# Optimization experiments

Hardware: AMD Instinct MI355X
Metric: run time of the kernel (lower is better)

Reference implementation:

```python
import jax, jax.numpy as jnp
import numpy as np

N, L, D, H, DFF = 16, 192, 512, 8, 2048
HD = D // H


def _mha(q, k, v, wq, bq, wk, bk, wv, bv, wo, bo, mask=None):
    # q: [B, Lq, D], k/v: [B, Lk, D]
    B, Lq, _ = q.shape
    def proj(x, W, b):
        y = x @ W + b
        return y.reshape(B, -1, H, HD).transpose(0, 2, 1, 3)  # [B, H, L, HD]
    Q, K, V = proj(q, wq, bq), proj(k, wk, bk), proj(v, wv, bv)
    QK = jnp.einsum('bhqd,bhkd->bhqk', Q, K) / jnp.sqrt(jnp.asarray(HD, Q.dtype))
    if mask is not None:
        QK = QK + (1.0 - mask) * (-1e9)
    A = jax.nn.softmax(QK, axis=-1)
    out = jnp.einsum('bhqk,bhkd->bhqd', A, V).transpose(0, 2, 1, 3).reshape(B, Lq, D)
    return out @ wo + bo


def _ln(x, g, b, eps=1e-6):
    mu = x.mean(-1, keepdims=True)
    var = ((x - mu) ** 2).mean(-1, keepdims=True)
    return (x - mu) / jnp.sqrt(var + eps) * g + b


def setup_inputs() -> dict:
    key = jax.random.key(0)
    ks = jax.random.split(key, 16)
    w = lambda k, sh: jax.random.normal(k, sh, jnp.float32) * 0.02
    inp = {
        'S': jax.random.normal(ks[0], (N, L, D), jnp.float32),
        'padding_mask': jax.random.randint(ks[1], (N * N, 1, 1, L), 0, 2, dtype=jnp.int32),
        'training': 0,
    }
    for i, nm in enumerate(['ca_wq', 'ca_wk', 'ca_wv', 'ca_wo', 'ia_wq', 'ia_wk', 'ia_wv', 'ia_wo']):
        inp[nm] = w(ks[2 + i], (D, D))
        inp[nm.replace('w', 'b')] = jnp.zeros((D,), jnp.float32)
    inp['ffn_w1'] = w(ks[10], (D, DFF)); inp['ffn_b1'] = jnp.zeros((DFF,), jnp.float32)
    inp['ffn_w2'] = w(ks[11], (DFF, D)); inp['ffn_b2'] = jnp.zeros((D,), jnp.float32)
    inp['ln1_g'] = jnp.ones((D,), jnp.float32); inp['ln1_b'] = jnp.zeros((D,), jnp.float32)
    inp['ln2_g'] = jnp.ones((D,), jnp.float32); inp['ln2_b'] = jnp.zeros((D,), jnp.float32)
    return inp


def reference(S, ca_wq, ca_bq, ca_wk, ca_bk, ca_wv, ca_bv, ca_wo, ca_bo,
              ia_wq, ia_bq, ia_wk, ia_bk, ia_wv, ia_bv, ia_wo, ia_bo,
              ffn_w1, ffn_b1, ffn_w2, ffn_b2, ln1_g, ln1_b, ln2_g, ln2_b,
              padding_mask, training):
    # training == 0 -> dropout layers are identity (inference mode)
    mask = padding_mask.astype(S.dtype)
    n, l, d = S.shape
    # all-pairs cross attention: query seq i attends to key/value seq j
    queries = jnp.repeat(S, n, axis=0)   # [n*n, l, d]
    keyvalue = jnp.tile(S, (n, 1, 1))    # [n*n, l, d]
    S_attn = _mha(queries, keyvalue, keyvalue,
                  ca_wq, ca_bq, ca_wk, ca_bk, ca_wv, ca_bv, ca_wo, ca_bo, mask=mask)
    S_attn = S_attn.reshape(n, n, l, d).transpose(1, 2, 0, 3).reshape(n * l, n, d)
    S_flip = S.reshape(n * l, 1, d)
    S_attn = _mha(S_flip, S_attn, S_attn,
                  ia_wq, ia_bq, ia_wk, ia_bk, ia_wv, ia_bv, ia_wo, ia_bo)
    S_attn = S_attn.reshape(n, l, d)
    S_norm = _ln(S + S_attn, ln1_g, ln1_b)
    S_ffn = jax.nn.relu(S_norm @ ffn_w1 + ffn_b1) @ ffn_w2 + ffn_b2
    return _ln(S_norm + S_ffn, ln2_g, ln2_b)
```

## Files before the change

### kernel.cpp

```cpp
#include <hip/hip_runtime.h>


using u16 = unsigned short;
using u32 = unsigned int;
typedef __attribute__((ext_vector_type(8))) short short8;
typedef __attribute__((ext_vector_type(4))) float f32x4;

__device__ __forceinline__ u32 cvtpk(float lo, float hi) {
  u32 r;
  asm("v_cvt_pk_bf16_f32 %0, %1, %2" : "=v"(r) : "v"(lo), "v"(hi));
  return r;
}
__device__ __forceinline__ u16 f2bf(float f) { return (u16)cvtpk(f, f); }
__device__ __forceinline__ float bf2f(u16 h) {
  return __uint_as_float(((u32)h) << 16);
}
__device__ __forceinline__ f32x4 mfma16(short8 a, short8 b, f32x4 c) {
  return __builtin_amdgcn_mfma_f32_16x16x32_bf16(a, b, c, 0, 0, 0);
}
__device__ __forceinline__ void gload16(const void* g, u16* l) {
  __builtin_amdgcn_global_load_lds(
      (const __attribute__((address_space(1))) void*)g,
      (__attribute__((address_space(3))) void*)l, 16, 0, 0);
}

template<int ROWS, int NT>
__device__ __forceinline__ void stage_g16(u16* lds, const u16* __restrict__ src,
                                          int ld, int tid) {
  constexpr int UNITS = ROWS * 8;
  constexpr int WV = NT / 64;
  int lane = tid & 63, w = tid >> 6;
  #pragma unroll
  for (int u = 0; u < UNITS / NT; ++u) {
    int base = (u * WV + w) * 64;
    int unit = base + lane;
    int row = unit >> 3, co = unit & 7;
    gload16(src + (long)row * ld + ((co ^ (row & 7)) << 3), lds + base * 8);
  }
}
template<int ROWS, int NT>
__device__ __forceinline__ void stage_f32(u16* lds, const float* __restrict__ src,
                                          int ld, int tid) {
  constexpr int UNITS = ROWS * 8;
  #pragma unroll
  for (int u = 0; u < UNITS / NT; ++u) {
    int unit = tid + u * NT;
    int row = unit >> 3, co = unit & 7;
    const float* g = src + (long)row * ld + (co << 3);
    float4 a = *(const float4*)g;
    float4 b = *(const float4*)(g + 4);
    u32 p[4] = {cvtpk(a.x, a.y), cvtpk(a.z, a.w),
                cvtpk(b.x, b.y), cvtpk(b.z, b.w)};
    *(uint4*)&lds[(row << 6) + ((co ^ (row & 7)) << 3)] = *(const uint4*)p;
  }
}

template<typename AT, typename BT, int BM, int BN, int WM, int WN>
__device__ __forceinline__ void gemm_core(const AT* __restrict__ A, int lda,
                                          const BT* __restrict__ Bt, int ldb, int K,
                                          u16* As, u16* Bs,
                                          f32x4 (&acc)[BM / (WM * 16)][BN / (WN * 16)]) {
  constexpr int NT = WM * WN * 64;
  constexpr int MI = BM / (WM * 16), NJ = BN / (WN * 16);
  int tid = threadIdx.x, lane = tid & 63, wid = tid >> 6;
  int wr = wid % WM, wc = wid / WM;
  int g = lane >> 4, c = lane & 15;
  #pragma unroll
  for (int mi = 0; mi < MI; ++mi)
    #pragma unroll
    for (int nj = 0; nj < NJ; ++nj)
      acc[mi][nj] = f32x4{0.f, 0.f, 0.f, 0.f};
  for (int kb = 0; kb < K; kb += 64) {
    __syncthreads();
    if constexpr (sizeof(AT) == 4) stage_f32<BM, NT>(As, A + kb, lda, tid);
    else                           stage_g16<BM, NT>(As, A + kb, lda, tid);
    if constexpr (sizeof(BT) == 4) stage_f32<BN, NT>(Bs, Bt + kb, ldb, tid);
    else                           stage_g16<BN, NT>(Bs, Bt + kb, ldb, tid);
    __syncthreads();
    #pragma unroll
    for (int kk = 0; kk < 2; ++kk) {
      int sl = ((kk * 4 + g) ^ (c & 7)) << 3;
      short8 af[MI], bfr[NJ];
      #pragma unroll
      for (int mi = 0; mi < MI; ++mi)
        af[mi] = *(const short8*)&As[((wr * (BM / WM) + mi * 16 + c) << 6) + sl];
      #pragma unroll
      for (int nj = 0; nj < NJ; ++nj)
        bfr[nj] = *(const short8*)&Bs[((wc * (BN / WN) + nj * 16 + c) << 6) + sl];
      #pragma unroll
      for (int mi = 0; mi < MI; ++mi)
        #pragma unroll
        for (int nj = 0; nj < NJ; ++nj)
          acc[mi][nj] = mfma16(af[mi], bfr[nj], acc[mi][nj]);
    }
  }
}

struct TJob { const float* src; u16* dst; int R, C, tile0; };
struct TJobs { TJob j[9]; };

__global__ __launch_bounds__(256) void k_transpose(TJobs jobs) {
  __shared__ float tile[32][33];
  int t = blockIdx.x;
  int ji = 0;
  #pragma unroll
  for (int k = 1; k < 9; ++k)
    if (t >= jobs.j[k].tile0) ji = k;
  TJob jb = jobs.j[ji];
  int lt = t - jb.tile0;
  int tpr = jb.C >> 5;
  int tr = lt / tpr, tc = lt % tpr;
  int tid = threadIdx.x;
  #pragma unroll
  for (int u = 0; u < 4; ++u) {
    int e = tid + u * 256;
    int r = e >> 5, cc = e & 31;
    tile[r][cc] = jb.src[(long)(tr * 32 + r) * jb.C + tc * 32 + cc];
  }
  __syncthreads();
  #pragma unroll
  for (int u = 0; u < 4; ++u) {
    int e = tid + u * 256;
    int r = e >> 5, cc = e & 31;
    jb.dst[(long)(tc * 32 + r) * jb.R + tr * 32 + cc] = f2bf(tile[cc][r]);
  }
}

__global__ __launch_bounds__(256) void k_qkv(const float* __restrict__ S,
    const u16* __restrict__ bt0, const u16* __restrict__ bt1,
    const u16* __restrict__ bt2, const u16* __restrict__ bt3,
    const float* __restrict__ b0, const float* __restrict__ b1,
    const float* __restrict__ b2, const float* __restrict__ b3,
    u16* __restrict__ Qc, u16* __restrict__ Kc, u16* __restrict__ Vt,
    u16* __restrict__ Qi) {
  __shared__ u16 As[128 * 64];
  __shared__ u16 Bs[128 * 64];
  int f = blockIdx.x;
  int swz = (f & 7) * 12 + (f >> 3);
  int mb = swz >> 2, nb = swz & 3, z = blockIdx.y;
  const u16* bt = z == 0 ? bt0 : z == 1 ? bt1 : z == 2 ? bt2 : bt3;
  const float* bias = z == 0 ? b0 : z == 1 ? b1 : z == 2 ? b2 : b3;
  f32x4 acc[4][4];
  gemm_core<float, u16, 128, 128, 2, 2>(S + (long)mb * 128 * 512, 512,
                                        bt + (long)nb * 128 * 512, 512, 512,
                                        As, Bs, acc);
  int lane = threadIdx.x & 63, wid = threadIdx.x >> 6;
  int wr = wid & 1, wc = wid >> 1, g = lane >> 4, cl = lane & 15;
  #pragma unroll
  for (int mi = 0; mi < 4; ++mi)
    #pragma unroll
    for (int nj = 0; nj < 4; ++nj)
      #pragma unroll
      for (int r = 0; r < 4; ++r) {
        int row = mb * 128 + wr * 64 + mi * 16 + g * 4 + r;
        int col = nb * 128 + wc * 64 + nj * 16 + cl;
        float v = acc[mi][nj][r] + bias[col];
        int seq = row / 192, t = row % 192, h = col >> 6, hd = col & 63;
        if (z == 0)      Qc[((long)(seq * 8 + h) * 192 + t) * 64 + hd] = f2bf(v * 0.125f);
        else if (z == 1) Kc[((long)(seq * 8 + h) * 192 + t) * 64 + hd] = f2bf(v);
        else if (z == 2) Vt[((long)(seq * 8 + h) * 64 + hd) * 192 + t] = f2bf(v);
        else             Qi[(long)row * 512 + col] = f2bf(v * 0.125f);
      }
}

__global__ __launch_bounds__(256) void k_attn_ca(const u16* __restrict__ Qc,
    const u16* __restrict__ Kc, const u16* __restrict__ VtG,
    const int* __restrict__ mask, u16* __restrict__ AC) {
  __shared__ u16 Ks[192 * 64];
  __shared__ u16 Vs[64 * 192];
  __shared__ __align__(16) float mbf[192];
  int bh = blockIdx.x;
  int b = bh >> 3, h = bh & 7;
  int i = b >> 4, j = b & 15;
  int tid = threadIdx.x, lane = tid & 63, w = tid >> 6;
  int g = lane >> 4, c = lane & 15;
  int qb = w * 48;

  const u16* Kbase = Kc + (long)(j * 8 + h) * 192 * 64;
  #pragma unroll
  for (int u = 0; u < 6; ++u) {
    int base = (u * 4 + w) * 64;
    int unit = base + lane;
    int row = unit >> 3, co = unit & 7;
    gload16(Kbase + (long)row * 64 + ((co ^ (row & 7)) << 3), Ks + base * 8);
  }
  const u16* Vbase = VtG + (long)(j * 8 + h) * 64 * 192;
  #pragma unroll
  for (int u = 0; u < 6; ++u) {
    int base = (u * 4 + w) * 64;
    int unit = base + lane;
    int row = unit / 24, co = unit - row * 24;
    gload16(Vbase + (long)row * 192 + ((co ^ (row & 7)) << 3), Vs + base * 8);
  }
  short8 bq[3][2];
  const u16* Qbase = Qc + (long)(i * 8 + h) * 192 * 64;
  #pragma unroll
  for (int nj = 0; nj < 3; ++nj)
    #pragma unroll
    for (int ks = 0; ks < 2; ++ks)
      bq[nj][ks] = *(const short8*)(Qbase + (long)(qb + nj * 16 + c) * 64 + ks * 32 + g * 8);
  if (tid < 192) mbf[tid] = mask[(long)b * 192 + tid] ? 0.f : -1e9f;
  __syncthreads();

  f32x4 oa[4][3];
  #pragma unroll
  for (int mi = 0; mi < 4; ++mi)
    #pragma unroll
    for (int nj = 0; nj < 3; ++nj)
      oa[mi][nj] = f32x4{0.f, 0.f, 0.f, 0.f};
  float sm[3] = {0.f, 0.f, 0.f};
  int srcLo = c | ((g & 1) << 5);
  int srcHi = srcLo + 16;
  int hi = g & 2;

  for (int s = 0; s < 6; ++s) {
    short8 ak[2][2];
    #pragma unroll
    for (int kh = 0; kh < 2; ++kh) {
      int row = (2 * s + kh) * 16 + c;
      #pragma unroll
      for (int ks = 0; ks < 2; ++ks)
        ak[kh][ks] = *(const short8*)&Ks[(row << 6) + (((ks * 4 + g) ^ (c & 7)) << 3)];
    }
    f32x4 sa[2][3];
    __builtin_amdgcn_s_setprio(1);
    #pragma unroll
    for (int kh = 0; kh < 2; ++kh)
      #pragma unroll
      for (int nj = 0; nj < 3; ++nj) {
        sa[kh][nj] = mfma16(ak[kh][0], bq[nj][0], f32x4{0.f, 0.f, 0.f, 0.f});
        sa[kh][nj] = mfma16(ak[kh][1], bq[nj][1], sa[kh][nj]);
      }
    __builtin_amdgcn_s_setprio(0);
    u32 pk[2][3][2];
    #pragma unroll
    for (int kh = 0; kh < 2; ++kh) {
      f32x4 m4 = *(const f32x4*)&mbf[(2 * s + kh) * 16 + g * 4];
      #pragma unroll
      for (int nj = 0; nj < 3; ++nj) {
        float p0 = __expf(sa[kh][nj][0] + m4[0]);
        float p1 = __expf(sa[kh][nj][1] + m4[1]);
        float p2 = __expf(sa[kh][nj][2] + m4[2]);
        float p3 = __expf(sa[kh][nj][3] + m4[3]);
        sm[nj] += (p0 + p1) + (p2 + p3);
        pk[kh][nj][0] = cvtpk(p0, p1);
        pk[kh][nj][1] = cvtpk(p2, p3);
      }
    }
    short8 bfg[3];
    #pragma unroll
    for (int nj = 0; nj < 3; ++nj) {
      u32 w0a = (u32)__shfl((int)pk[0][nj][0], srcLo);
      u32 w0b = (u32)__shfl((int)pk[1][nj][0], srcLo);
      u32 w1a = (u32)__shfl((int)pk[0][nj][1], srcLo);
      u32 w1b = (u32)__shfl((int)pk[1][nj][1], srcLo);
      u32 w2a = (u32)__shfl((int)pk[0][nj][0], srcHi);
      u32 w2b = (u32)__shfl((int)pk[1][nj][0], srcHi);
      u32 w3a = (u32)__shfl((int)pk[0][nj][1], srcHi);
      u32 w3b = (u32)__shfl((int)pk[1][nj][1], srcHi);
      union { u32 u[4]; short8 s8; } bf;
      bf.u[0] = hi ? w0b : w0a;
      bf.u[1] = hi ? w1b : w1a;
      bf.u[2] = hi ? w2b : w2a;
      bf.u[3] = hi ? w3b : w3a;
      bfg[nj] = bf.s8;
    }
    int sl = ((s * 4 + g) ^ (c & 7)) << 3;
    __builtin_amdgcn_s_setprio(1);
    #pragma unroll
    for (int mi = 0; mi < 4; ++mi) {
      short8 av = *(const short8*)&Vs[(mi * 16 + c) * 192 + sl];
      #pragma unroll
      for (int nj = 0; nj < 3; ++nj)
        oa[mi][nj] = mfma16(av, bfg[nj], oa[mi][nj]);
    }
    __builtin_amdgcn_s_setprio(0);
  }
  #pragma unroll
  for (int nj = 0; nj < 3; ++nj) {
    sm[nj] += __shfl_xor(sm[nj], 16);
    sm[nj] += __shfl_xor(sm[nj], 32);
  }
  #pragma unroll
  for (int nj = 0; nj < 3; ++nj) {
    float rs = 1.0f / sm[nj];
    int q = qb + nj * 16 + c;
    u16* dst = AC + ((long)(b * 192 + q)) * 512 + h * 64 + g * 4;
    #pragma unroll
    for (int mi = 0; mi < 4; ++mi) {
      u32 p2[2] = {cvtpk(oa[mi][nj][0] * rs, oa[mi][nj][1] * rs),
                   cvtpk(oa[mi][nj][2] * rs, oa[mi][nj][3] * rs)};
      *(uint2*)(dst + mi * 16) = *(const uint2*)p2;
    }
  }
}

__global__ __launch_bounds__(256) void k_oproj_ca(const u16* __restrict__ AC,
    const u16* __restrict__ woT, const float* __restrict__ bo,
    u16* __restrict__ S2) {
  __shared__ u16 As[128 * 64];
  __shared__ u16 Bs[128 * 64];
  int f = blockIdx.x;
  int swz = (f & 7) * 192 + (f >> 3);
  int mb = swz >> 2, nb = swz & 3;
  f32x4 acc[4][4];
  gemm_core<u16, u16, 128, 128, 2, 2>(AC + (long)mb * 128 * 512, 512,
                                      woT + (long)nb * 128 * 512, 512, 512,
                                      As, Bs, acc);
  int lane = threadIdx.x & 63, wid = threadIdx.x >> 6;
  int wr = wid & 1, wc = wid >> 1, g = lane >> 4, cl = lane & 15;
  #pragma unroll
  for (int mi = 0; mi < 4; ++mi)
    #pragma unroll
    for (int nj = 0; nj < 4; ++nj)
      #pragma unroll
      for (int r = 0; r < 4; ++r) {
        int row = mb * 128 + wr * 64 + mi * 16 + g * 4 + r;
        int col = nb * 128 + wc * 64 + nj * 16 + cl;
        S2[(long)row * 512 + col] = f2bf(acc[mi][nj][r] + bo[col]);
      }
}

__global__ __launch_bounds__(256) void k_uproj(const u16* __restrict__ Qi,
    const float* __restrict__ wk, u16* __restrict__ U) {
  __shared__ u16 As[128 * 64];
  __shared__ u16 Bs[128 * 64];
  int mb = blockIdx.x, nb = blockIdx.y, h = blockIdx.z;
  f32x4 acc[4][4];
  gemm_core<u16, float, 128, 128, 2, 2>(Qi + (long)mb * 128 * 512 + h * 64, 512,
                                        wk + (long)nb * 128 * 512 + h * 64, 512, 64,
                                        As, Bs, acc);
  int lane = threadIdx.x & 63, wid = threadIdx.x >> 6;
  int wr = wid & 1, wc = wid >> 1, g = lane >> 4, cl = lane & 15;
  #pragma unroll
  for (int mi = 0; mi < 4; ++mi)
    #pragma unroll
    for (int nj = 0; nj < 4; ++nj)
      #pragma unroll
      for (int r = 0; r < 4; ++r) {
        int row = mb * 128 + wr * 64 + mi * 16 + g * 4 + r;
        int col = nb * 128 + wc * 64 + nj * 16 + cl;
        U[((long)row * 8 + h) * 512 + col] = f2bf(acc[mi][nj][r]);
      }
}

__global__ __launch_bounds__(256) void k_ia_attn(const u16* __restrict__ S2,
    const u16* __restrict__ U, const u16* __restrict__ Qi,
    const float* __restrict__ bk, u16* __restrict__ Y) {
  __shared__ u16 s2[16 * 520];
  __shared__ float Lp[4][16][17];
  __shared__ float aL[8][16];
  __shared__ float cL[8];
  int tok = blockIdx.x;
  int tid = threadIdx.x, lane = tid & 63, w = tid >> 6;
  {
    const u16* src = S2 + (long)tok * 512;
    #pragma unroll
    for (int u = 0; u < 4; ++u) {
      int e = tid + u * 256;
      int r = e >> 6, cc = (e & 63) << 3;
      *(uint4*)&s2[r * 520 + cc] = *(const uint4*)(src + (long)r * 3072 * 512 + cc);
    }
  }
  if (w == 0) {
    int h = lane >> 3, p = lane & 7;
    short8 qv = *(const short8*)(Qi + (long)tok * 512 + h * 64 + p * 8);
    const float* bkp = bk + h * 64 + p * 8;
    float s = 0.f;
    #pragma unroll
    for (int v = 0; v < 8; ++v) s += bf2f((u16)qv[v]) * bkp[v];
    s += __shfl_xor(s, 1); s += __shfl_xor(s, 2); s += __shfl_xor(s, 4);
    if (p == 0) cL[h] = s;
  }
  __syncthreads();
  {
    int g = lane >> 4, c = lane & 15;
    const u16* Ub = U + (long)tok * 4096 + (long)(c & 7) * 512;
    f32x4 accL = {0.f, 0.f, 0.f, 0.f};
    #pragma unroll
    for (int kk = 0; kk < 4; ++kk) {
      int d = w * 128 + kk * 32 + g * 8;
      short8 aS = *(const short8*)&s2[c * 520 + d];
      short8 bU = *(const short8*)(Ub + d);
      accL = mfma16(aS, bU, accL);
    }
    #pragma unroll
    for (int r = 0; r < 4; ++r) Lp[w][g * 4 + r][c] = accL[r];
  }
  __syncthreads();
  if (w == 0) {
    int h = lane & 7, i0 = lane >> 3;
    float L0 = Lp[0][i0][h] + Lp[1][i0][h] + Lp[2][i0][h] + Lp[3][i0][h] + cL[h];
    float L1 = Lp[0][i0 + 8][h] + Lp[1][i0 + 8][h] + Lp[2][i0 + 8][h] +
               Lp[3][i0 + 8][h] + cL[h];
    float e0 = __expf(L0), e1 = __expf(L1);
    float s = e0 + e1;
    s += __shfl_xor(s, 8); s += __shfl_xor(s, 16); s += __shfl_xor(s, 32);
    float rs = 1.0f / s;
    aL[h][i0] = e0 * rs;
    aL[h][i0 + 8] = e1 * rs;
  }
  __syncthreads();
  {
    int h = tid & 7, d0 = (tid >> 3) << 4;
    float y[16];
    #pragma unroll
    for (int v = 0; v < 16; ++v) y[v] = 0.f;
    #pragma unroll
    for (int i = 0; i < 16; ++i) {
      float a = aL[h][i];
      short8 v0 = *(const short8*)&s2[i * 520 + d0];
      short8 v1 = *(const short8*)&s2[i * 520 + d0 + 8];
      #pragma unroll
      for (int v = 0; v < 8; ++v) {
        y[v]     += a * bf2f((u16)v0[v]);
        y[8 + v] += a * bf2f((u16)v1[v]);
      }
    }
    u32 o[8];
    #pragma unroll
    for (int v = 0; v < 8; ++v) o[v] = cvtpk(y[2 * v], y[2 * v + 1]);
    u16* dst = Y + ((long)tok * 8 + h) * 512 + d0;
    *(uint4*)dst = *(const uint4*)&o[0];
    *(uint4*)(dst + 8) = *(const uint4*)&o[4];
  }
}

__global__ __launch_bounds__(256) void k_vapply(const u16* __restrict__ Y,
    const u16* __restrict__ wvT, const float* __restrict__ bv,
    u16* __restrict__ AO) {
  __shared__ u16 As[128 * 64];
  __shared__ u16 Bs[64 * 64];
  int mb = blockIdx.x, h = blockIdx.z;
  f32x4 acc[2][4];
  gemm_core<u16, u16, 128, 64, 4, 1>(Y + (long)mb * 128 * 4096 + h * 512, 4096,
                                     wvT + (long)h * 64 * 512, 512, 512,
                                     As, Bs, acc);
  int lane = threadIdx.x & 63, wid = threadIdx.x >> 6;
  int g = lane >> 4, cl = lane & 15;
  #pragma unroll
  for (int mi = 0; mi < 2; ++mi)
    #pragma unroll
    for (int nj = 0; nj < 4; ++nj)
      #pragma unroll
      for (int r = 0; r < 4; ++r) {
        int row = mb * 128 + wid * 32 + mi * 16 + g * 4 + r;
        int col = h * 64 + nj * 16 + cl;
        AO[(long)row * 512 + col] = f2bf(acc[mi][nj][r] + bv[col]);
      }
}

__global__ __launch_bounds__(256) void k_gemm_f32out(const u16* __restrict__ A, int K,
    const u16* __restrict__ BT, const float* __restrict__ bias,
    float* __restrict__ out) {
  __shared__ u16 As[128 * 64];
  __shared__ u16 Bs[64 * 64];
  int f = blockIdx.x;
  int swz = (f & 7) * 24 + (f >> 3);
  int mb = swz >> 3, nb = swz & 7;
  f32x4 acc[4][2];
  gemm_core<u16, u16, 128, 64, 2, 2>(A + (long)mb * 128 * K, K,
                                     BT + (long)nb * 64 * K, K, K, As, Bs, acc);
  int lane = threadIdx.x & 63, wid = threadIdx.x >> 6;
  int wr = wid & 1, wc = wid >> 1, g = lane >> 4, cl = lane & 15;
  #pragma unroll
  for (int mi = 0; mi < 4; ++mi)
    #pragma unroll
    for (int nj = 0; nj < 2; ++nj)
      #pragma unroll
      for (int r = 0; r < 4; ++r) {
        int row = mb * 128 + wr * 64 + mi * 16 + g * 4 + r;
        int col = nb * 64 + wc * 32 + nj * 16 + cl;
        out[(long)row * 512 + col] = acc[mi][nj][r] + bias[col];
      }
}

__global__ __launch_bounds__(256) void k_ffn1(const u16* __restrict__ A,
    const u16* __restrict__ BT, const float* __restrict__ bias,
    u16* __restrict__ out) {
  __shared__ u16 As[128 * 64];
  __shared__ u16 Bs[128 * 64];
  int f = blockIdx.x;
  int swz = (f & 7) * 48 + (f >> 3);
  int mb = swz >> 4, nb = swz & 15;
  f32x4 acc[4][4];
  gemm_core<u16, u16, 128, 128, 2, 2>(A + (long)mb * 128 * 512, 512,
                                      BT + (long)nb * 128 * 512, 512, 512,
                                      As, Bs, acc);
  int lane = threadIdx.x & 63, wid = threadIdx.x >> 6;
  int wr = wid & 1, wc = wid >> 1, g = lane >> 4, cl = lane & 15;
  #pragma unroll
  for (int mi = 0; mi < 4; ++mi)
    #pragma unroll
    for (int nj = 0; nj < 4; ++nj)
      #pragma unroll
      for (int r = 0; r < 4; ++r) {
        int row = mb * 128 + wr * 64 + mi * 16 + g * 4 + r;
        int col = nb * 128 + wc * 64 + nj * 16 + cl;
        out[(long)row * 2048 + col] = f2bf(fmaxf(acc[mi][nj][r] + bias[col], 0.f));
      }
}

__global__ __launch_bounds__(256) void k_ln(const float* __restrict__ X1,
    const float* __restrict__ X2, const float* __restrict__ gg,
    const float* __restrict__ bb, float* __restrict__ outF,
    u16* __restrict__ outB) {
  __shared__ float red[8];
  int row = blockIdx.x, tid = threadIdx.x;
  long base = (long)row * 512;
  float x0 = X1[base + tid] + X2[base + tid];
  float x1 = X1[base + tid + 256] + X2[base + tid + 256];
  float s = x0 + x1, ss = x0 * x0 + x1 * x1;
  #pragma unroll
  for (int m = 1; m <= 32; m <<= 1) {
    s += __shfl_xor(s, m);
    ss += __shfl_xor(ss, m);
  }
  int w = tid >> 6;
  if ((tid & 63) == 0) { red[w] = s; red[4 + w] = ss; }
  __syncthreads();
  s = red[0] + red[1] + red[2] + red[3];
  ss = red[4] + red[5] + red[6] + red[7];
  float mu = s * (1.0f / 512.0f);
  float var = ss * (1.0f / 512.0f) - mu * mu;
  float rstd = 1.0f / sqrtf(var + 1e-6f);
  float y0 = (x0 - mu) * rstd * gg[tid] + bb[tid];
  float y1 = (x1 - mu) * rstd * gg[tid + 256] + bb[tid + 256];
  if (outF) { outF[base + tid] = y0; outF[base + tid + 256] = y1; }
  if (outB) { outB[base + tid] = f2bf(y0); outB[base + tid + 256] = f2bf(y1); }
}

extern "C" void kernel_launch(void* const* d_in, const int* in_sizes, int n_in,
                              void* d_out, int out_size, void* d_ws, size_t ws_size,
                              hipStream_t stream) {
  const float* S      = (const float*)d_in[0];
  const int*   maskp  = (const int*)d_in[1];
  const float* ca_wq  = (const float*)d_in[3];
  const float* ca_bq  = (const float*)d_in[4];
  const float* ca_wk  = (const float*)d_in[5];
  const float* ca_bk  = (const float*)d_in[6];
  const float* ca_wv  = (const float*)d_in[7];
  const float* ca_bv  = (const float*)d_in[8];
  const float* ca_wo  = (const float*)d_in[9];
  const float* ca_bo  = (const float*)d_in[10];
  const float* ia_wq  = (const float*)d_in[11];
  const float* ia_bq  = (const float*)d_in[12];
  const float* ia_wk  = (const float*)d_in[13];
  const float* ia_bk  = (const float*)d_in[14];
  const float* ia_wv  = (const float*)d_in[15];
  const float* ia_bv  = (const float*)d_in[16];
  const float* ia_wo  = (const float*)d_in[17];
  const float* ia_bo  = (const float*)d_in[18];
  const float* ffn_w1 = (const float*)d_in[19];
  const float* ffn_b1 = (const float*)d_in[20];
  const float* ffn_w2 = (const float*)d_in[21];
  const float* ffn_b2 = (const float*)d_in[22];
  const float* ln1_g  = (const float*)d_in[23];
  const float* ln1_b  = (const float*)d_in[24];
  const float* ln2_g  = (const float*)d_in[25];
  const float* ln2_b  = (const float*)d_in[26];

  char* ws = (char*)d_ws;
  constexpr size_t OFF_WQT  = 0;
  constexpr size_t OFF_WKT  = 524288;
  constexpr size_t OFF_WVT  = 1048576;
  constexpr size_t OFF_IQT  = 1572864;
  constexpr size_t OFF_WOTC = 2097152;
  constexpr size_t OFF_WVTI = 2621440;
  constexpr size_t OFF_WOTI = 3145728;
  constexpr size_t OFF_W1T  = 3670016;
  constexpr size_t OFF_W2T  = 5767168;
  constexpr size_t OFF_QC   = 7864320;
  constexpr size_t OFF_KC   = 11010048;
  constexpr size_t OFF_VT   = 14155776;
  constexpr size_t OFF_QI   = 17301504;
  constexpr size_t OFF_AC   = 20447232;
  constexpr size_t OFF_S2   = 70778880;
  constexpr size_t OFF_U    = OFF_AC;
  constexpr size_t OFF_Y    = OFF_AC + 25165824;
  constexpr size_t OFF_AO   = OFF_QI;
  constexpr size_t OFF_IAO  = OFF_QC;
  constexpr size_t OFF_SNB  = OFF_VT;
  constexpr size_t OFF_SNF  = OFF_S2;
  constexpr size_t OFF_HFF  = OFF_S2 + 6291456;
  constexpr size_t OFF_FFO  = OFF_HFF + 12582912;

  u16* wqT  = (u16*)(ws + OFF_WQT);
  u16* wkT  = (u16*)(ws + OFF_WKT);
  u16* wvT  = (u16*)(ws + OFF_WVT);
  u16* iqT  = (u16*)(ws + OFF_IQT);
  u16* woTc = (u16*)(ws + OFF_WOTC);
  u16* wvTi = (u16*)(ws + OFF_WVTI);
  u16* woTi = (u16*)(ws + OFF_WOTI);
  u16* w1T  = (u16*)(ws + OFF_W1T);
  u16* w2T  = (u16*)(ws + OFF_W2T);
  u16* Qc   = (u16*)(ws + OFF_QC);
  u16* Kc   = (u16*)(ws + OFF_KC);
  u16* Vt   = (u16*)(ws + OFF_VT);
  u16* Qi   = (u16*)(ws + OFF_QI);
  u16* AC   = (u16*)(ws + OFF_AC);
  u16* S2   = (u16*)(ws + OFF_S2);
  u16* U    = (u16*)(ws + OFF_U);
  u16* Y    = (u16*)(ws + OFF_Y);
  u16* AO   = (u16*)(ws + OFF_AO);
  float* IAO = (float*)(ws + OFF_IAO);
  u16* SNB  = (u16*)(ws + OFF_SNB);
  float* SNF = (float*)(ws + OFF_SNF);
  u16* HFF  = (u16*)(ws + OFF_HFF);
  float* FFO = (float*)(ws + OFF_FFO);

  TJobs tj;
  int t0 = 0;
  auto SET = [&](int k, const float* s, u16* d, int R, int C) {
    tj.j[k].src = s; tj.j[k].dst = d; tj.j[k].R = R; tj.j[k].C = C; tj.j[k].tile0 = t0;
    t0 += (R / 32) * (C / 32);
  };
  SET(0, ca_wq, wqT, 512, 512);
  SET(1, ca_wk, wkT, 512, 512);
  SET(2, ca_wv, wvT, 512, 512);
  SET(3, ia_wq, iqT, 512, 512);
  SET(4, ca_wo, woTc, 512, 512);
  SET(5, ia_wv, wvTi, 512, 512);
  SET(6, ia_wo, woTi, 512, 512);
  SET(7, ffn_w1, w1T, 512, 2048);
  SET(8, ffn_w2, w2T, 2048, 512);

  k_transpose<<<dim3(t0), 256, 0, stream>>>(tj);
  k_qkv<<<dim3(96, 4), 256, 0, stream>>>(S, wqT, wkT, wvT, iqT,
                                         ca_bq, ca_bk, ca_bv, ia_bq,
                                         Qc, Kc, Vt, Qi);
  k_attn_ca<<<dim3(2048), 256, 0, stream>>>(Qc, Kc, Vt, maskp, AC);
  k_oproj_ca<<<dim3(1536), 256, 0, stream>>>(AC, woTc, ca_bo, S2);
  k_uproj<<<dim3(24, 4, 8), 256, 0, stream>>>(Qi, ia_wk, U);
  k_ia_attn<<<dim3(3072), 256, 0, stream>>>(S2, U, Qi, ia_bk, Y);
  k_vapply<<<dim3(24, 1, 8), 256, 0, stream>>>(Y, wvTi, ia_bv, AO);
  k_gemm_f32out<<<dim3(192), 256, 0, stream>>>(AO, 512, woTi, ia_bo, IAO);
  k_ln<<<dim3(3072), 256, 0, stream>>>(S, IAO, ln1_g, ln1_b, SNF, SNB);
  k_ffn1<<<dim3(384), 256, 0, stream>>>(SNB, w1T, ffn_b1, HFF);
  k_gemm_f32out<<<dim3(192), 256, 0, stream>>>(HFF, 2048, w2T, ffn_b2, FFO);
  k_ln<<<dim3(3072), 256, 0, stream>>>(SNF, FFO, ln2_g, ln2_b, (float*)d_out, nullptr);
}
```

Baseline: 210.8 us.

## Pre-cast S to bf16, merge QKV launches, co-schedule attention with U projection

Adds a kernel that casts S to bf16 once, so the QKV GEMM reads bf16 instead of converting fp32 in each of its four z-slices. The four projection weights are stored contiguously and k_qkv runs as one 1D grid over all 16 column blocks. When the workspace is large enough, the cross-attention blocks and the U-projection GEMM blocks share one launch, removing a kernel boundary and filling idle CUs. The cost is an extra cast kernel, a larger workspace footprint, and a merged kernel that needs the larger shared-memory allocation for both paths.

```diff
diff --git a/kernel.cpp b/kernel.cpp
--- a/kernel.cpp
+++ b/kernel.cpp
@@ -96,6 +96,16 @@
   }
 }
 
+__global__ __launch_bounds__(256) void k_cast(const float* __restrict__ S,
+                                              u16* __restrict__ Sb) {
+  int idx = (blockIdx.x * 256 + threadIdx.x) * 8;
+  float4 a = *(const float4*)(S + idx);
+  float4 b = *(const float4*)(S + idx + 4);
+  u32 p[4] = {cvtpk(a.x, a.y), cvtpk(a.z, a.w),
+              cvtpk(b.x, b.y), cvtpk(b.z, b.w)};
+  *(uint4*)(Sb + idx) = *(const uint4*)p;
+}
+
 struct TJob { const float* src; u16* dst; int R, C, tile0; };
 struct TJobs { TJob j[9]; };
 
@@ -126,24 +136,23 @@
   }
 }
 
-__global__ __launch_bounds__(256) void k_qkv(const float* __restrict__ S,
-    const u16* __restrict__ bt0, const u16* __restrict__ bt1,
-    const u16* __restrict__ bt2, const u16* __restrict__ bt3,
+__global__ __launch_bounds__(256) void k_qkv(const u16* __restrict__ Sb,
+    const u16* __restrict__ btAll,
     const float* __restrict__ b0, const float* __restrict__ b1,
     const float* __restrict__ b2, const float* __restrict__ b3,
     u16* __restrict__ Qc, u16* __restrict__ Kc, u16* __restrict__ Vt,
     u16* __restrict__ Qi) {
-  __shared__ u16 As[128 * 64];
-  __shared__ u16 Bs[128 * 64];
+  __shared__ u16 SH[16384];
   int f = blockIdx.x;
-  int swz = (f & 7) * 12 + (f >> 3);
-  int mb = swz >> 2, nb = swz & 3, z = blockIdx.y;
-  const u16* bt = z == 0 ? bt0 : z == 1 ? bt1 : z == 2 ? bt2 : bt3;
+  int swz = (f & 7) * 48 + (f >> 3);
+  int mb = swz >> 4, nb = swz & 15;
+  f32x4 acc[4][4];
+  gemm_core<u16, u16, 128, 128, 2, 2>(Sb + (long)mb * 128 * 512, 512,
+                                      btAll + (long)nb * 128 * 512, 512, 512,
+                                      SH, SH + 8192, acc);
+  int z = nb >> 2;
   const float* bias = z == 0 ? b0 : z == 1 ? b1 : z == 2 ? b2 : b3;
-  f32x4 acc[4][4];
-  gemm_core<float, u16, 128, 128, 2, 2>(S + (long)mb * 128 * 512, 512,
-                                        bt + (long)nb * 128 * 512, 512, 512,
-                                        As, Bs, acc);
+  float scale = (z == 0 || z == 3) ? 0.125f : 1.0f;
   int lane = threadIdx.x & 63, wid = threadIdx.x >> 6;
   int wr = wid & 1, wc = wid >> 1, g = lane >> 4, cl = lane & 15;
   #pragma unroll
@@ -153,145 +162,171 @@
       #pragma unroll
       for (int r = 0; r < 4; ++r) {
         int row = mb * 128 + wr * 64 + mi * 16 + g * 4 + r;
-        int col = nb * 128 + wc * 64 + nj * 16 + cl;
-        float v = acc[mi][nj][r] + bias[col];
-        int seq = row / 192, t = row % 192, h = col >> 6, hd = col & 63;
-        if (z == 0)      Qc[((long)(seq * 8 + h) * 192 + t) * 64 + hd] = f2bf(v * 0.125f);
+        int cz = (nb & 3) * 128 + wc * 64 + nj * 16 + cl;
+        float v = (acc[mi][nj][r] + bias[cz]) * scale;
+        int seq = row / 192, t = row % 192, h = cz >> 6, hd = cz & 63;
+        if (z == 0)      Qc[((long)(seq * 8 + h) * 192 + t) * 64 + hd] = f2bf(v);
         else if (z == 1) Kc[((long)(seq * 8 + h) * 192 + t) * 64 + hd] = f2bf(v);
         else if (z == 2) Vt[((long)(seq * 8 + h) * 64 + hd) * 192 + t] = f2bf(v);
-        else             Qi[(long)row * 512 + col] = f2bf(v * 0.125f);
-      }
-}
-
-__global__ __launch_bounds__(256) void k_attn_ca(const u16* __restrict__ Qc,
+        else             Qi[(long)row * 512 + cz] = f2bf(v);
+      }
+}
+
+__global__ __launch_bounds__(256) void k_attn_up(const u16* __restrict__ Qc,
     const u16* __restrict__ Kc, const u16* __restrict__ VtG,
-    const int* __restrict__ mask, u16* __restrict__ AC) {
-  __shared__ u16 Ks[192 * 64];
-  __shared__ u16 Vs[64 * 192];
-  __shared__ __align__(16) float mbf[192];
-  int bh = blockIdx.x;
-  int b = bh >> 3, h = bh & 7;
-  int i = b >> 4, j = b & 15;
+    const int* __restrict__ mask, u16* __restrict__ AC,
+    const u16* __restrict__ Qi, const float* __restrict__ wk,
+    u16* __restrict__ U, int attnBlocks) {
+  __shared__ __align__(16) u16 SH[24960];
+  int bid = blockIdx.x;
   int tid = threadIdx.x, lane = tid & 63, w = tid >> 6;
   int g = lane >> 4, c = lane & 15;
-  int qb = w * 48;
-
-  const u16* Kbase = Kc + (long)(j * 8 + h) * 192 * 64;
-  #pragma unroll
-  for (int u = 0; u < 6; ++u) {
-    int base = (u * 4 + w) * 64;
-    int unit = base + lane;
-    int row = unit >> 3, co = unit & 7;
-    gload16(Kbase + (long)row * 64 + ((co ^ (row & 7)) << 3), Ks + base * 8);
-  }
-  const u16* Vbase = VtG + (long)(j * 8 + h) * 64 * 192;
-  #pragma unroll
-  for (int u = 0; u < 6; ++u) {
-    int base = (u * 4 + w) * 64;
-    int unit = base + lane;
-    int row = unit / 24, co = unit - row * 24;
-    gload16(Vbase + (long)row * 192 + ((co ^ (row & 7)) << 3), Vs + base * 8);
-  }
-  short8 bq[3][2];
-  const u16* Qbase = Qc + (long)(i * 8 + h) * 192 * 64;
-  #pragma unroll
-  for (int nj = 0; nj < 3; ++nj)
-    #pragma unroll
-    for (int ks = 0; ks < 2; ++ks)
-      bq[nj][ks] = *(const short8*)(Qbase + (long)(qb + nj * 16 + c) * 64 + ks * 32 + g * 8);
-  if (tid < 192) mbf[tid] = mask[(long)b * 192 + tid] ? 0.f : -1e9f;
-  __syncthreads();
-
-  f32x4 oa[4][3];
-  #pragma unroll
-  for (int mi = 0; mi < 4; ++mi)
+  if (bid < attnBlocks) {
+    u16* Ks = SH;
+    u16* Vs = SH + 12288;
+    float* mbf = (float*)(SH + 24576);
+    int b = bid >> 3, h = bid & 7;
+    int i = b >> 4, j = b & 15;
+    int qb = w * 48;
+
+    const u16* Kbase = Kc + (long)(j * 8 + h) * 192 * 64;
+    #pragma unroll
+    for (int u = 0; u < 6; ++u) {
+      int base = (u * 4 + w) * 64;
+      int unit = base + lane;
+      int row = unit >> 3, co = unit & 7;
+      gload16(Kbase + (long)row * 64 + ((co ^ (row & 7)) << 3), Ks + base * 8);
+    }
+    const u16* Vbase = VtG + (long)(j * 8 + h) * 64 * 192;
+    #pragma unroll
+    for (int u = 0; u < 6; ++u) {
+      int base = (u * 4 + w) * 64;
+      int unit = base + lane;
+      int row = unit / 24, co = unit - row * 24;
+      gload16(Vbase + (long)row * 192 + ((co ^ (row & 7)) << 3), Vs + base * 8);
+    }
+    short8 bq[3][2];
+    const u16* Qbase = Qc + (long)(i * 8 + h) * 192 * 64;
     #pragma unroll
     for (int nj = 0; nj < 3; ++nj)
-      oa[mi][nj] = f32x4{0.f, 0.f, 0.f, 0.f};
-  float sm[3] = {0.f, 0.f, 0.f};
-  int srcLo = c | ((g & 1) << 5);
-  int srcHi = srcLo + 16;
-  int hi = g & 2;
-
-  for (int s = 0; s < 6; ++s) {
-    short8 ak[2][2];
-    #pragma unroll
-    for (int kh = 0; kh < 2; ++kh) {
-      int row = (2 * s + kh) * 16 + c;
       #pragma unroll
       for (int ks = 0; ks < 2; ++ks)
-        ak[kh][ks] = *(const short8*)&Ks[(row << 6) + (((ks * 4 + g) ^ (c & 7)) << 3)];
-    }
-    f32x4 sa[2][3];
-    __builtin_amdgcn_s_setprio(1);
-    #pragma unroll
-    for (int kh = 0; kh < 2; ++kh)
+        bq[nj][ks] = *(const short8*)(Qbase + (long)(qb + nj * 16 + c) * 64 + ks * 32 + g * 8);
+    if (tid < 192) mbf[tid] = mask[(long)b * 192 + tid] ? 0.f : -1e9f;
+    __syncthreads();
+
+    f32x4 oa[4][3];
+    #pragma unroll
+    for (int mi = 0; mi < 4; ++mi)
+      #pragma unroll
+      for (int nj = 0; nj < 3; ++nj)
+        oa[mi][nj] = f32x4{0.f, 0.f, 0.f, 0.f};
+    float sm[3] = {0.f, 0.f, 0.f};
+    int srcLo = c | ((g & 1) << 5);
+    int srcHi = srcLo + 16;
+    int hi = g & 2;
+
+    for (int s = 0; s < 6; ++s) {
+      short8 ak[2][2];
+      #pragma unroll
+      for (int kh = 0; kh < 2; ++kh) {
+        int row = (2 * s + kh) * 16 + c;
+        #pragma unroll
+        for (int ks = 0; ks < 2; ++ks)
+          ak[kh][ks] = *(const short8*)&Ks[(row << 6) + (((ks * 4 + g) ^ (c & 7)) << 3)];
+      }
+      f32x4 sa[2][3];
+      __builtin_amdgcn_s_setprio(1);
+      #pragma unroll
+      for (int kh = 0; kh < 2; ++kh)
+        #pragma unroll
+        for (int nj = 0; nj < 3; ++nj) {
+          sa[kh][nj] = mfma16(ak[kh][0], bq[nj][0], f32x4{0.f, 0.f, 0.f, 0.f});
+          sa[kh][nj] = mfma16(ak[kh][1], bq[nj][1], sa[kh][nj]);
+        }
+      __builtin_amdgcn_s_setprio(0);
+      u32 pk[2][3][2];
+      #pragma unroll
+      for (int kh = 0; kh < 2; ++kh) {
+        f32x4 m4 = *(const f32x4*)&mbf[(2 * s + kh) * 16 + g * 4];
+        #pragma unroll
+        for (int nj = 0; nj < 3; ++nj) {
+          float p0 = __expf(sa[kh][nj][0] + m4[0]);
+          float p1 = __expf(sa[kh][nj][1] + m4[1]);
+          float p2 = __expf(sa[kh][nj][2] + m4[2]);
+          float p3 = __expf(sa[kh][nj][3] + m4[3]);
+          sm[nj] += (p0 + p1) + (p2 + p3);
+          pk[kh][nj][0] = cvtpk(p0, p1);
+          pk[kh][nj][1] = cvtpk(p2, p3);
+        }
+      }
+      short8 bfg[3];
       #pragma unroll
       for (int nj = 0; nj < 3; ++nj) {
-        sa[kh][nj] = mfma16(ak[kh][0], bq[nj][0], f32x4{0.f, 0.f, 0.f, 0.f});
-        sa[kh][nj] = mfma16(ak[kh][1], bq[nj][1], sa[kh][nj]);
-      }
-    __builtin_amdgcn_s_setprio(0);
-    u32 pk[2][3][2];
-    #pragma unroll
-    for (int kh = 0; kh < 2; ++kh) {
-      f32x4 m4 = *(const f32x4*)&mbf[(2 * s + kh) * 16 + g * 4];
-      #pragma unroll
-      for (int nj = 0; nj < 3; ++nj) {
-        float p0 = __expf(sa[kh][nj][0] + m4[0]);
-        float p1 = __expf(sa[kh][nj][1] + m4[1]);
-        float p2 = __expf(sa[kh][nj][2] + m4[2]);
-        float p3 = __expf(sa[kh][nj][3] + m4[3]);
-        sm[nj] += (p0 + p1) + (p2 + p3);
-        pk[kh][nj][0] = cvtpk(p0, p1);
-        pk[kh][nj][1] = cvtpk(p2, p3);
-      }
-    }
-    short8 bfg[3];
+        u32 w0a = (u32)__shfl((int)pk[0][nj][0], srcLo);
+        u32 w0b = (u32)__shfl((int)pk[1][nj][0], srcLo);
+        u32 w1a = (u32)__shfl((int)pk[0][nj][1], srcLo);
+        u32 w1b = (u32)__shfl((int)pk[1][nj][1], srcLo);
+        u32 w2a = (u32)__shfl((int)pk[0][nj][0], srcHi);
+        u32 w2b = (u32)__shfl((int)pk[1][nj][0], srcHi);
+        u32 w3a = (u32)__shfl((int)pk[0][nj][1], srcHi);
+        u32 w3b = (u32)__shfl((int)pk[1][nj][1], srcHi);
+        union { u32 u[4]; short8 s8; } bf;
+        bf.u[0] = hi ? w0b : w0a;
+        bf.u[1] = hi ? w1b : w1a;
+        bf.u[2] = hi ? w2b : w2a;
+        bf.u[3] = hi ? w3b : w3a;
+        bfg[nj] = bf.s8;
+      }
+      int sl = ((s * 4 + g) ^ (c & 7)) << 3;
+      __builtin_amdgcn_s_setprio(1);
+      #pragma unroll
+      for (int mi = 0; mi < 4; ++mi) {
+        short8 av = *(const short8*)&Vs[(mi * 16 + c) * 192 + sl];
+        #pragma unroll
+        for (int nj = 0; nj < 3; ++nj)
+          oa[mi][nj] = mfma16(av, bfg[nj], oa[mi][nj]);
+      }
+      __builtin_amdgcn_s_setprio(0);
+    }
     #pragma unroll
     for (int nj = 0; nj < 3; ++nj) {
-      u32 w0a = (u32)__shfl((int)pk[0][nj][0], srcLo);
-      u32 w0b = (u32)__shfl((int)pk[1][nj][0], srcLo);
-      u32 w1a = (u32)__shfl((int)pk[0][nj][1], srcLo);
-      u32 w1b = (u32)__shfl((int)pk[1][nj][1], srcLo);
-      u32 w2a = (u32)__shfl((int)pk[0][nj][0], srcHi);
-      u32 w2b = (u32)__shfl((int)pk[1][nj][0], srcHi);
-      u32 w3a = (u32)__shfl((int)pk[0][nj][1], srcHi);
-      u32 w3b = (u32)__shfl((int)pk[1][nj][1], srcHi);
-      union { u32 u[4]; short8 s8; } bf;
-      bf.u[0] = hi ? w0b : w0a;
-      bf.u[1] = hi ? w1b : w1a;
-      bf.u[2] = hi ? w2b : w2a;
-      bf.u[3] = hi ? w3b : w3a;
-      bfg[nj] = bf.s8;
-    }
-    int sl = ((s * 4 + g) ^ (c & 7)) << 3;
-    __builtin_amdgcn_s_setprio(1);
-    #pragma unroll
-    for (int mi = 0; mi < 4; ++mi) {
-      short8 av = *(const short8*)&Vs[(mi * 16 + c) * 192 + sl];
-      #pragma unroll
-      for (int nj = 0; nj < 3; ++nj)
-        oa[mi][nj] = mfma16(av, bfg[nj], oa[mi][nj]);
-    }
-    __builtin_amdgcn_s_setprio(0);
-  }
-  #pragma unroll
-  for (int nj = 0; nj < 3; ++nj) {
-    sm[nj] += __shfl_xor(sm[nj], 16);
-    sm[nj] += __shfl_xor(sm[nj], 32);
-  }
-  #pragma unroll
-  for (int nj = 0; nj < 3; ++nj) {
-    float rs = 1.0f / sm[nj];
-    int q = qb + nj * 16 + c;
-    u16* dst = AC + ((long)(b * 192 + q)) * 512 + h * 64 + g * 4;
-    #pragma unroll
-    for (int mi = 0; mi < 4; ++mi) {
-      u32 p2[2] = {cvtpk(oa[mi][nj][0] * rs, oa[mi][nj][1] * rs),
-                   cvtpk(oa[mi][nj][2] * rs, oa[mi][nj][3] * rs)};
-      *(uint2*)(dst + mi * 16) = *(const uint2*)p2;
-    }
+      sm[nj] += __shfl_xor(sm[nj], 16);
+      sm[nj] += __shfl_xor(sm[nj], 32);
+    }
+    #pragma unroll
+    for (int nj = 0; nj < 3; ++nj) {
+      float rs = 1.0f / sm[nj];
+      int q = qb + nj * 16 + c;
+      u16* dst = AC + ((long)(b * 192 + q)) * 512 + h * 64 + g * 4;
+      #pragma unroll
+      for (int mi = 0; mi < 4; ++mi) {
+        u32 p2[2] = {cvtpk(oa[mi][nj][0] * rs, oa[mi][nj][1] * rs),
+                     cvtpk(oa[mi][nj][2] * rs, oa[mi][nj][3] * rs)};
+        *(uint2*)(dst + mi * 16) = *(const uint2*)p2;
+      }
+    }
+  } else {
+    u16* As = SH;
+    u16* Bs = SH + 8192;
+    int t = bid - attnBlocks;
+    int mb = t % 24, r2 = t / 24;
+    int nb = r2 & 3, h = r2 >> 2;
+    f32x4 acc[4][4];
+    gemm_core<u16, float, 128, 128, 2, 2>(Qi + (long)mb * 128 * 512 + h * 64, 512,
+                                          wk + (long)nb * 128 * 512 + h * 64, 512, 64,
+                                          As, Bs, acc);
+    int wr = w & 1, wc = w >> 1, cl = lane & 15;
+    #pragma unroll
+    for (int mi = 0; mi < 4; ++mi)
+      #pragma unroll
+      for (int nj = 0; nj < 4; ++nj)
+        #pragma unroll
+        for (int r = 0; r < 4; ++r) {
+          int row = mb * 128 + wr * 64 + mi * 16 + g * 4 + r;
+          int col = nb * 128 + wc * 64 + nj * 16 + cl;
+          U[((long)row * 8 + h) * 512 + col] = f2bf(acc[mi][nj][r]);
+        }
   }
 }
 
@@ -318,29 +353,6 @@
         int row = mb * 128 + wr * 64 + mi * 16 + g * 4 + r;
         int col = nb * 128 + wc * 64 + nj * 16 + cl;
         S2[(long)row * 512 + col] = f2bf(acc[mi][nj][r] + bo[col]);
-      }
-}
-
-__global__ __launch_bounds__(256) void k_uproj(const u16* __restrict__ Qi,
-    const float* __restrict__ wk, u16* __restrict__ U) {
-  __shared__ u16 As[128 * 64];
-  __shared__ u16 Bs[128 * 64];
-  int mb = blockIdx.x, nb = blockIdx.y, h = blockIdx.z;
-  f32x4 acc[4][4];
-  gemm_core<u16, float, 128, 128, 2, 2>(Qi + (long)mb * 128 * 512 + h * 64, 512,
-                                        wk + (long)nb * 128 * 512 + h * 64, 512, 64,
-                                        As, Bs, acc);
-  int lane = threadIdx.x & 63, wid = threadIdx.x >> 6;
-  int wr = wid & 1, wc = wid >> 1, g = lane >> 4, cl = lane & 15;
-  #pragma unroll
-  for (int mi = 0; mi < 4; ++mi)
-    #pragma unroll
-    for (int nj = 0; nj < 4; ++nj)
-      #pragma unroll
-      for (int r = 0; r < 4; ++r) {
-        int row = mb * 128 + wr * 64 + mi * 16 + g * 4 + r;
-        int col = nb * 128 + wc * 64 + nj * 16 + cl;
-        U[((long)row * 8 + h) * 512 + col] = f2bf(acc[mi][nj][r]);
       }
 }
 
@@ -562,9 +574,6 @@
 
   char* ws = (char*)d_ws;
   constexpr size_t OFF_WQT  = 0;
-  constexpr size_t OFF_WKT  = 524288;
-  constexpr size_t OFF_WVT  = 1048576;
-  constexpr size_t OFF_IQT  = 1572864;
   constexpr size_t OFF_WOTC = 2097152;
   constexpr size_t OFF_WVTI = 2621440;
   constexpr size_t OFF_WOTI = 3145728;
@@ -576,7 +585,9 @@
   constexpr size_t OFF_QI   = 17301504;
   constexpr size_t OFF_AC   = 20447232;
   constexpr size_t OFF_S2   = 70778880;
-  constexpr size_t OFF_U    = OFF_AC;
+  constexpr size_t OFF_UBIG = 121110528;
+  constexpr size_t NEED_BIG = OFF_UBIG + 25165824;
+  constexpr size_t OFF_SB   = OFF_AC;
   constexpr size_t OFF_Y    = OFF_AC + 25165824;
   constexpr size_t OFF_AO   = OFF_QI;
   constexpr size_t OFF_IAO  = OFF_QC;
@@ -586,9 +597,6 @@
   constexpr size_t OFF_FFO  = OFF_HFF + 12582912;
 
   u16* wqT  = (u16*)(ws + OFF_WQT);
-  u16* wkT  = (u16*)(ws + OFF_WKT);
-  u16* wvT  = (u16*)(ws + OFF_WVT);
-  u16* iqT  = (u16*)(ws + OFF_IQT);
   u16* woTc = (u16*)(ws + OFF_WOTC);
   u16* wvTi = (u16*)(ws + OFF_WVTI);
   u16* woTi = (u16*)(ws + OFF_WOTI);
@@ -599,8 +607,8 @@
   u16* Vt   = (u16*)(ws + OFF_VT);
   u16* Qi   = (u16*)(ws + OFF_QI);
   u16* AC   = (u16*)(ws + OFF_AC);
+  u16* Sb   = (u16*)(ws + OFF_SB);
   u16* S2   = (u16*)(ws + OFF_S2);
-  u16* U    = (u16*)(ws + OFF_U);
   u16* Y    = (u16*)(ws + OFF_Y);
   u16* AO   = (u16*)(ws + OFF_AO);
   float* IAO = (float*)(ws + OFF_IAO);
@@ -609,6 +617,9 @@
   u16* HFF  = (u16*)(ws + OFF_HFF);
   float* FFO = (float*)(ws + OFF_FFO);
 
+  bool bigws = ws_size >= NEED_BIG;
+  u16* U = bigws ? (u16*)(ws + OFF_UBIG) : (u16*)(ws + OFF_AC);
+
   TJobs tj;
   int t0 = 0;
   auto SET = [&](int k, const float* s, u16* d, int R, int C) {
@@ -616,22 +627,30 @@
     t0 += (R / 32) * (C / 32);
   };
   SET(0, ca_wq, wqT, 512, 512);
-  SET(1, ca_wk, wkT, 512, 512);
-  SET(2, ca_wv, wvT, 512, 512);
-  SET(3, ia_wq, iqT, 512, 512);
+  SET(1, ca_wk, wqT + 262144, 512, 512);
+  SET(2, ca_wv, wqT + 524288, 512, 512);
+  SET(3, ia_wq, wqT + 786432, 512, 512);
   SET(4, ca_wo, woTc, 512, 512);
   SET(5, ia_wv, wvTi, 512, 512);
   SET(6, ia_wo, woTi, 512, 512);
   SET(7, ffn_w1, w1T, 512, 2048);
   SET(8, ffn_w2, w2T, 2048, 512);
 
+  k_cast<<<dim3(768), 256, 0, stream>>>(S, Sb);
   k_transpose<<<dim3(t0), 256, 0, stream>>>(tj);
-  k_qkv<<<dim3(96, 4), 256, 0, stream>>>(S, wqT, wkT, wvT, iqT,
-                                         ca_bq, ca_bk, ca_bv, ia_bq,
-                                         Qc, Kc, Vt, Qi);
-  k_attn_ca<<<dim3(2048), 256, 0, stream>>>(Qc, Kc, Vt, maskp, AC);
-  k_oproj_ca<<<dim3(1536), 256, 0, stream>>>(AC, woTc, ca_bo, S2);
-  k_uproj<<<dim3(24, 4, 8), 256, 0, stream>>>(Qi, ia_wk, U);
+  k_qkv<<<dim3(384), 256, 0, stream>>>(Sb, wqT, ca_bq, ca_bk, ca_bv, ia_bq,
+                                       Qc, Kc, Vt, Qi);
+  if (bigws) {
+    k_attn_up<<<dim3(2816), 256, 0, stream>>>(Qc, Kc, Vt, maskp, AC, Qi, ia_wk,
+                                              U, 2048);
+    k_oproj_ca<<<dim3(1536), 256, 0, stream>>>(AC, woTc, ca_bo, S2);
+  } else {
+    k_attn_up<<<dim3(2048), 256, 0, stream>>>(Qc, Kc, Vt, maskp, AC, Qi, ia_wk,
+                                              U, 2048);
+    k_oproj_ca<<<dim3(1536), 256, 0, stream>>>(AC, woTc, ca_bo, S2);
+    k_attn_up<<<dim3(768), 256, 0, stream>>>(Qc, Kc, Vt, maskp, AC, Qi, ia_wk,
+                                             U, 0);
+  }
   k_ia_attn<<<dim3(3072), 256, 0, stream>>>(S2, U, Qi, ia_bk, Y);
   k_vapply<<<dim3(24, 1, 8), 256, 0, stream>>>(Y, wvTi, ia_bv, AO);
   k_gemm_f32out<<<dim3(192), 256, 0, stream>>>(AO, 512, woTi, ia_bo, IAO);
```

Result: no change. 209.5 us (-0.6%).
